# Optimization experiments

Hardware: AMD Instinct MI355X
Metric: run time of the kernel (lower is better)

The kernel has to match this reference:

```python
import jax, jax.numpy as jnp
import numpy as np

B, S, D = 2, 2048, 2048
H, DH, DR = 16, 128, 64
DC_KV, DC_Q = 512, 1536
ROPE_BASE = 10000.0


def _rope(t):
    """Apply rotate-half RoPE over the last dim of t: [B, S, H, DR]."""
    s, dr = t.shape[1], t.shape[-1]
    inv_freq = 1.0 / (ROPE_BASE ** (jnp.arange(0, dr, 2, dtype=jnp.float32) / dr))
    ang = jnp.arange(s, dtype=jnp.float32)[:, None] * inv_freq  # [S, DR/2]
    cos = jnp.tile(jnp.cos(ang), (1, 2))[None, :, None, :]  # [1,S,1,DR]
    sin = jnp.tile(jnp.sin(ang), (1, 2))[None, :, None, :]
    t1, t2 = jnp.split(t, 2, axis=-1)
    rot = jnp.concatenate([-t2, t1], axis=-1)
    return t * cos + rot * sin


def setup_inputs() -> dict:
    key = jax.random.key(0)
    ks = jax.random.split(key, 18)
    g = lambda k, shp: (jax.random.normal(k, shp, dtype=jnp.float32) * 0.02)
    return {
        "x": jax.random.normal(ks[0], (B, S, D), dtype=jnp.float32),
        "Wkd": g(ks[1], (DC_KV, D)),   "bkd": jnp.zeros((DC_KV,), jnp.float32),
        "Wqd": g(ks[2], (DC_Q, D)),    "bqd": jnp.zeros((DC_Q,), jnp.float32),
        "Wku": g(ks[3], (H * DH, DC_KV)), "bku": jnp.zeros((H * DH,), jnp.float32),
        "Wvu": g(ks[4], (H * DH, DC_KV)), "bvu": jnp.zeros((H * DH,), jnp.float32),
        "Wqu": g(ks[5], (H * DH, DC_Q)),  "bqu": jnp.zeros((H * DH,), jnp.float32),
        "Wkr": g(ks[6], (H * DR, D)),     "bkr": jnp.zeros((H * DR,), jnp.float32),
        "Wqr": g(ks[7], (H * DR, DC_Q)),  "bqr": jnp.zeros((H * DR,), jnp.float32),
        "Wo": g(ks[8], (D, H * DH)),      "bo": jnp.zeros((D,), jnp.float32),
    }


def reference(x, Wkd, bkd, Wqd, bqd, Wku, bku, Wvu, bvu, Wqu, bqu,
              Wkr, bkr, Wqr, bqr, Wo, bo):
    b, s, _ = x.shape
    # 1. Compress to latent spaces
    kv_c = x @ Wkd.T + bkd          # [B,S,DC_KV]
    q_c = x @ Wqd.T + bqd           # [B,S,DC_Q]
    # 2-3. Up-project content / value / rope features
    k_cnt = (kv_c @ Wku.T + bku).reshape(b, s, H, DH)
    v = (kv_c @ Wvu.T + bvu).reshape(b, s, H, DH)
    q_cnt = (q_c @ Wqu.T + bqu).reshape(b, s, H, DH)
    k_r = (x @ Wkr.T + bkr).reshape(b, s, H, DR)      # keys rope from input (eq. 3)
    q_r = (q_c @ Wqr.T + bqr).reshape(b, s, H, DR)    # query rope from latent (eq. 8)
    # 5. Partial RoPE: rotate position features, concat with content
    q_full = jnp.concatenate([q_cnt, _rope(q_r)], axis=-1)  # [B,S,H,DH+DR]
    k_full = jnp.concatenate([k_cnt, _rope(k_r)], axis=-1)
    # 7. Manual causal attention (mscale = 1)
    scale = 1.0 / jnp.sqrt(jnp.float32(DH + DR))
    scores = jnp.einsum("bqhd,bkhd->bhqk", q_full, k_full) * scale
    causal = jnp.tril(jnp.ones((s, s), dtype=bool))
    scores = jnp.where(causal[None, None], scores, jnp.float32(-1e9))
    probs = jax.nn.softmax(scores, axis=-1)
    attn = jnp.einsum("bhqk,bkhd->bqhd", probs, v).reshape(b, s, H * DH)
    # 9. Output projection
    return attn @ Wo.T + bo
```

## Files before the change

kernel.cpp:

```cpp
#include <hip/hip_runtime.h>
#include <stdint.h>
#include <stddef.h>

#define BB 2
#define SS 2048
#define DD 2048
#define HH 16
#define DHH 128
#define DRR 64
#define DCKV 512
#define DCQ 1536

typedef __attribute__((ext_vector_type(8))) short short8;
typedef __attribute__((ext_vector_type(4))) short short4v;
typedef __attribute__((ext_vector_type(4))) float f32x4;
typedef unsigned int u32;

__device__ __forceinline__ short f2bf(float x) {
  unsigned u = __float_as_uint(x);
  u += 0x7fffu + ((u >> 16) & 1u);
  return (short)(u >> 16);
}
__device__ __forceinline__ float bf2f(short s) {
  return __uint_as_float(((unsigned)(unsigned short)s) << 16);
}

#define BAR_NOVM() asm volatile("s_waitcnt lgkmcnt(0)\n\ts_barrier" ::: "memory")

__device__ __forceinline__ void gl2lds16(const short* g, short* l) {
  __builtin_amdgcn_global_load_lds(
      (const __attribute__((address_space(1))) u32*)g,
      (__attribute__((address_space(3))) u32*)l, 16, 0, 0);
}

__global__ __launch_bounds__(256) void cast_bf16_kernel(const float* __restrict__ in,
                                                        short* __restrict__ out, int n4) {
  int i = blockIdx.x * 256 + threadIdx.x;
  if (i >= n4) return;
  f32x4 f = ((const f32x4*)in)[i];
  short4v o;
  o[0] = f2bf(f[0]); o[1] = f2bf(f[1]); o[2] = f2bf(f[2]); o[3] = f2bf(f[3]);
  ((short4v*)out)[i] = o;
}

__global__ __launch_bounds__(256) void concat_bias_kernel(
    const float* bkd, const float* bqd, const float* bkr,
    const float* bqu, const float* bqr, const float* bku, const float* bvu,
    float* cb1, float* cb2, float* cb3) {
  int idx = blockIdx.x * 256 + threadIdx.x;
  if (idx < 3072) {
    cb1[idx] = idx < 512 ? bkd[idx] : (idx < 2048 ? bqd[idx - 512] : bkr[idx - 2048]);
  } else if (idx < 6144) {
    int j = idx - 3072;
    cb2[j] = j < 2048 ? bqu[j] : bqr[j - 2048];
  } else if (idx < 10240) {
    int j = idx - 6144;
    cb3[j] = j < 2048 ? bku[j] : bvu[j - 2048];
  }
}

template<int MODE>
__global__ __launch_bounds__(256) void gemm_bt(const short* __restrict__ A, int lda,
                                               const short* __restrict__ Bm, int ldb,
                                               const float* __restrict__ bias,
                                               void* __restrict__ Cout, void* __restrict__ out2,
                                               int M, int N, int K) {
  __shared__ __align__(16) short sA[128 * 32];
  __shared__ __align__(16) short sB[128 * 32];
  const int tid = threadIdx.x;
  const int w = tid >> 6, L = tid & 63, quad = L >> 4, lc = L & 15;
  const int wm = w >> 1, wn = w & 1;
  const int tm = blockIdx.x * 128, tn = blockIdx.y * 128;
  const int lrow = L >> 2, lch = (L & 3) * 8;
  f32x4 acc[4][4] = {};
  const int nk = K >> 5;
  for (int kt = 0; kt < nk; ++kt) {
    const int k0 = kt << 5;
    __syncthreads();
    {
      int sub = w * 2;
      gl2lds16(A + (size_t)(tm + sub * 16 + lrow) * lda + k0 + lch, &sA[sub * 512]);
      gl2lds16(A + (size_t)(tm + sub * 16 + 16 + lrow) * lda + k0 + lch, &sA[sub * 512 + 512]);
      gl2lds16(Bm + (size_t)(tn + sub * 16 + lrow) * ldb + k0 + lch, &sB[sub * 512]);
      gl2lds16(Bm + (size_t)(tn + sub * 16 + 16 + lrow) * ldb + k0 + lch, &sB[sub * 512 + 512]);
    }
    __syncthreads();
    short8 af[4], bfr[4];
#pragma unroll
    for (int ms = 0; ms < 4; ++ms)
      af[ms] = *(const short8*)&sA[(wm * 64 + ms * 16 + lc) * 32 + quad * 8];
#pragma unroll
    for (int ns = 0; ns < 4; ++ns)
      bfr[ns] = *(const short8*)&sB[(wn * 64 + ns * 16 + lc) * 32 + quad * 8];
#pragma unroll
    for (int ms = 0; ms < 4; ++ms)
#pragma unroll
      for (int ns = 0; ns < 4; ++ns)
        acc[ms][ns] = __builtin_amdgcn_mfma_f32_16x16x32_bf16(af[ms], bfr[ns], acc[ms][ns], 0, 0, 0);
  }
#pragma unroll
  for (int ms = 0; ms < 4; ++ms) {
    int row = tm + wm * 64 + ms * 16 + quad * 4;
#pragma unroll
    for (int ns = 0; ns < 4; ++ns) {
      int col = tn + wn * 64 + ns * 16 + lc;
      float bv = bias[col];
      if (MODE == 3 && col >= 2048) {
        int j = col - 2048, h_ = j >> 7, dh = j & 127;
        int b_ = row >> 11, s0 = row & 2047;
        short4v pk;
#pragma unroll
        for (int r = 0; r < 4; ++r) pk[r] = f2bf(acc[ms][ns][r] + bv);
        *(short4v*)((short*)out2 + (((size_t)(b_ * HH + h_)) * DHH + dh) * SS + s0) = pk;
      } else {
#pragma unroll
        for (int r = 0; r < 4; ++r) {
          float vv = acc[ms][ns][r] + bv;
          int rrow = row + r;
          if (MODE == 0)      ((short*)Cout)[(size_t)rrow * N + col] = f2bf(vv);
          else if (MODE == 1) ((float*)Cout)[(size_t)rrow * N + col] = vv;
          else {
            if (col < 2048) {
              int b_ = rrow >> 11, s_ = rrow & 2047, h_ = col >> 7, d_ = col & 127;
              ((short*)Cout)[(((size_t)(b_ * HH + h_)) * SS + s_) * 192 + d_] = f2bf(vv);
            } else {
              ((short*)out2)[(size_t)rrow * 1024 + (col - 2048)] = f2bf(vv);
            }
          }
        }
      }
    }
  }
}

__global__ __launch_bounds__(256) void rope_kernel(const short* __restrict__ rin,
                                                   int rstride, int roff,
                                                   short* __restrict__ full) {
  int idx = blockIdx.x * 256 + threadIdx.x;
  int i = idx & 31, h = (idx >> 5) & 15, s = (idx >> 9) & 2047, b = idx >> 20;
  const short* base = rin + ((size_t)(b * SS + s)) * rstride + roff + h * DRR;
  float t1 = bf2f(base[i]), t2 = bf2f(base[i + 32]);
  float invf = expf(-9.210340371976184f * (float)i * (1.0f / 32.0f));
  float ang = (float)s * invf;
  float c = cosf(ang), sn = sinf(ang);
  short* ob = full + (((size_t)(b * HH + h)) * SS + s) * 192 + 128;
  ob[i]      = f2bf(t1 * c - t2 * sn);
  ob[i + 32] = f2bf(t1 * sn + t2 * c);
}

__device__ __forceinline__ float quad_max(float v) {
  v = fmaxf(v, __shfl_xor(v, 1));
  v = fmaxf(v, __shfl_xor(v, 2));
  v = fmaxf(v, __shfl_xor(v, 4));
  v = fmaxf(v, __shfl_xor(v, 8));
  return v;
}
__device__ __forceinline__ float quad_sum(float v) {
  v += __shfl_xor(v, 1); v += __shfl_xor(v, 2);
  v += __shfl_xor(v, 4); v += __shfl_xor(v, 8);
  return v;
}

__global__ __launch_bounds__(256, 2) void mla_flash_kernel(const short* __restrict__ Qf,
                                                           const short* __restrict__ Kf,
                                                           const short* __restrict__ Vt,
                                                           float* __restrict__ Opart,
                                                           float* __restrict__ Mpart,
                                                           float* __restrict__ Lpart,
                                                           short* __restrict__ attn) {
  const int bid = blockIdx.x;
  const int g0 = (bid & 7) * 160 + (bid >> 3);
  const int bh = g0 / 40, xc = g0 - bh * 40;
  int qt, c;
  if (xc < 4)       { qt = xc;                  c = 0; }
  else if (xc < 12) { qt = 4 + ((xc - 4) >> 1);  c = (xc - 4) & 1; }
  else if (xc < 24) { qt = 8 + (xc - 12) / 3;    c = (xc - 12) % 3; }
  else              { qt = 12 + ((xc - 24) >> 2); c = (xc - 24) & 3; }
  const int nc = (qt + 4) >> 2;
  const int k8 = c * 8;
  const int klim = 2 * qt + 2;
  const int kend = (k8 + 8 < klim) ? k8 + 8 : klim;
  const int slot = bh * 40 + xc;

  const int h = bh & 15, b = bh >> 4;
  const int tid = threadIdx.x, w = tid >> 6, L = tid & 63, quad = L >> 4, lc = L & 15;
  __shared__ __align__(16) short sK[12288];
  __shared__ __align__(16) short sV[8192];
  __shared__ __align__(16) short Pf[8192];

  const short* Qb = Qf + ((size_t)bh) * SS * 192;
  const short* Kb = Kf + ((size_t)bh) * SS * 192;
  const short* Vb = Vt + ((size_t)bh) * DHH * SS;

  const int qrow0 = qt * 128 + w * 32;
  short8 qa[2][6];
#pragma unroll
  for (int ms = 0; ms < 2; ++ms)
#pragma unroll
    for (int kk = 0; kk < 6; ++kk)
      qa[ms][kk] = *(const short8*)(Qb + (size_t)(qrow0 + ms * 16 + lc) * 192 + kk * 32 + quad * 8);

  f32x4 O[2][8] = {};
  float mrow[2][4], lrow[2][4];
#pragma unroll
  for (int ms = 0; ms < 2; ++ms)
#pragma unroll
    for (int r = 0; r < 4; ++r) { mrow[ms][r] = -1e30f; lrow[ms][r] = 0.f; }

  const int srow_ = tid >> 2, sq_ = tid & 3;
  const int sslot = srow_ * 4 + (sq_ ^ ((srow_ >> 1) & 3));
  const int vrow_ = tid >> 3, vch_ = tid & 7;
  short8 g[6], gv[4];
#pragma unroll
  for (int i = 0; i < 6; ++i)
    g[i] = *(const short8*)(Kb + (size_t)(k8 * 64 + srow_) * 192 + i * 32 + sq_ * 8);
#pragma unroll
  for (int j = 0; j < 4; ++j)
    gv[j] = *(const short8*)(Vb + (size_t)(j * 32 + vrow_) * SS + k8 * 64 + vch_ * 8);

  for (int kt = k8; kt < kend; ++kt) {
    BAR_NOVM();
#pragma unroll
    for (int i = 0; i < 6; ++i)
      *(short8*)&sK[(i * 256 + sslot) * 8] = g[i];
#pragma unroll
    for (int j = 0; j < 4; ++j) {
      int row = j * 32 + vrow_;
      *(short8*)&sV[row * 64 + ((vch_ ^ (row & 7)) << 3)] = gv[j];
    }
    if (kt + 1 < kend) {
#pragma unroll
      for (int i = 0; i < 6; ++i)
        g[i] = *(const short8*)(Kb + (size_t)((kt + 1) * 64 + srow_) * 192 + i * 32 + sq_ * 8);
#pragma unroll
      for (int j = 0; j < 4; ++j)
        gv[j] = *(const short8*)(Vb + (size_t)(j * 32 + vrow_) * SS + (kt + 1) * 64 + vch_ * 8);
    }
    BAR_NOVM();
    f32x4 sc[2][4] = {};
#pragma unroll
    for (int kk = 0; kk < 6; ++kk)
#pragma unroll
      for (int ns = 0; ns < 4; ++ns) {
        int rr = ns * 16 + lc;
        short8 kb = *(const short8*)&sK[(kk * 256 + rr * 4 + (quad ^ ((rr >> 1) & 3))) * 8];
        sc[0][ns] = __builtin_amdgcn_mfma_f32_16x16x32_bf16(qa[0][kk], kb, sc[0][ns], 0, 0, 0);
        sc[1][ns] = __builtin_amdgcn_mfma_f32_16x16x32_bf16(qa[1][kk], kb, sc[1][ns], 0, 0, 0);
      }
    const float scale = 0.07216878364870322f;
#pragma unroll
    for (int ms = 0; ms < 2; ++ms)
#pragma unroll
      for (int ns = 0; ns < 4; ++ns)
#pragma unroll
        for (int r = 0; r < 4; ++r) {
          float vv = sc[ms][ns][r] * scale;
          if (kt * 64 + ns * 16 + lc > qrow0 + ms * 16 + quad * 4 + r) vv = -1e30f;
          sc[ms][ns][r] = vv;
        }
#pragma unroll
    for (int ms = 0; ms < 2; ++ms)
#pragma unroll
      for (int r = 0; r < 4; ++r) {
        float mx = fmaxf(fmaxf(sc[ms][0][r], sc[ms][1][r]), fmaxf(sc[ms][2][r], sc[ms][3][r]));
        mx = quad_max(mx);
        float mnew = fmaxf(mrow[ms][r], mx);
        float alpha = __expf(mrow[ms][r] - mnew);
        mrow[ms][r] = mnew;
        float ps = 0.f;
#pragma unroll
        for (int ns = 0; ns < 4; ++ns) {
          float p = __expf(sc[ms][ns][r] - mnew);
          sc[ms][ns][r] = p;
          ps += p;
        }
        ps = quad_sum(ps);
        lrow[ms][r] = lrow[ms][r] * alpha + ps;
#pragma unroll
        for (int n = 0; n < 8; ++n) O[ms][n][r] *= alpha;
      }
#pragma unroll
    for (int ms = 0; ms < 2; ++ms)
#pragma unroll
      for (int ns = 0; ns < 4; ++ns)
#pragma unroll
        for (int r = 0; r < 4; ++r) {
          int row = w * 32 + ms * 16 + quad * 4 + r;
          int col = ns * 16 + lc;
          Pf[row * 64 + (((col >> 3) ^ (row & 7)) << 3) + (col & 7)] = f2bf(sc[ms][ns][r]);
        }
#pragma unroll
    for (int kk2 = 0; kk2 < 2; ++kk2) {
      int r0 = w * 32 + lc, r1 = w * 32 + 16 + lc;
      short8 pa0 = *(const short8*)&Pf[r0 * 64 + (((kk2 * 4 + quad) ^ (r0 & 7)) << 3)];
      short8 pa1 = *(const short8*)&Pf[r1 * 64 + (((kk2 * 4 + quad) ^ (r1 & 7)) << 3)];
      short8 vb[8];
#pragma unroll
      for (int n = 0; n < 8; ++n) {
        int rr = n * 16 + lc;
        vb[n] = *(const short8*)&sV[rr * 64 + (((kk2 * 4 + quad) ^ (lc & 7)) << 3)];
      }
#pragma unroll
      for (int n = 0; n < 8; ++n) {
        O[0][n] = __builtin_amdgcn_mfma_f32_16x16x32_bf16(pa0, vb[n], O[0][n], 0, 0, 0);
        O[1][n] = __builtin_amdgcn_mfma_f32_16x16x32_bf16(pa1, vb[n], O[1][n], 0, 0, 0);
      }
    }
  }
  if (nc == 1) {
#pragma unroll
    for (int ms = 0; ms < 2; ++ms)
#pragma unroll
      for (int r = 0; r < 4; ++r) {
        float inv = 1.0f / lrow[ms][r];
        int srow = qt * 128 + w * 32 + ms * 16 + quad * 4 + r;
        short* dst = attn + ((size_t)b * SS + srow) * 2048 + h * 128;
#pragma unroll
        for (int n = 0; n < 8; ++n)
          dst[n * 16 + lc] = f2bf(O[ms][n][r] * inv);
      }
  } else {
    float* Ob = Opart + (size_t)slot * 16384;
#pragma unroll
    for (int ms = 0; ms < 2; ++ms)
#pragma unroll
      for (int r = 0; r < 4; ++r) {
        int row = w * 32 + ms * 16 + quad * 4 + r;
#pragma unroll
        for (int n = 0; n < 8; ++n)
          Ob[(size_t)row * 128 + n * 16 + lc] = O[ms][n][r];
      }
    if (lc == 0) {
#pragma unroll
      for (int ms = 0; ms < 2; ++ms)
#pragma unroll
        for (int r = 0; r < 4; ++r) {
          int row = w * 32 + ms * 16 + quad * 4 + r;
          Mpart[slot * 128 + row] = mrow[ms][r];
          Lpart[slot * 128 + row] = lrow[ms][r];
        }
    }
  }
}

__global__ __launch_bounds__(256) void combine_kernel(const float* __restrict__ Op,
                                                      const float* __restrict__ Mp,
                                                      const float* __restrict__ Lp,
                                                      short* __restrict__ attn) {
  int idx = blockIdx.x * 256 + threadIdx.x;
  int col = idx & 127;
  int r = (idx >> 7) & 127;
  int t = idx >> 14;
  int bh = t / 12, qt = (t - bh * 12) + 4;
  int nc = (qt + 4) >> 2;
  int cbase;
  if (qt < 8)       cbase = 4 + 2 * (qt - 4);
  else if (qt < 12) cbase = 12 + 3 * (qt - 8);
  else              cbase = 24 + 4 * (qt - 12);
  int slot0 = bh * 40 + cbase;
  float mc[4];
#pragma unroll
  for (int cc = 0; cc < 4; ++cc)
    mc[cc] = (cc < nc) ? Mp[(size_t)(slot0 + cc) * 128 + r] : -1e30f;
  float M = fmaxf(fmaxf(mc[0], mc[1]), fmaxf(mc[2], mc[3]));
  float den = 0.f, acc = 0.f;
#pragma unroll
  for (int cc = 0; cc < 4; ++cc) {
    if (cc < nc) {
      float e = __expf(mc[cc] - M);
      den += e * Lp[(size_t)(slot0 + cc) * 128 + r];
      acc += e * Op[(size_t)(slot0 + cc) * 16384 + (size_t)r * 128 + col];
    }
  }
  int b = bh >> 4, hh = bh & 15;
  int srow = qt * 128 + r;
  attn[((size_t)b * SS + srow) * 2048 + hh * 128 + col] = f2bf(acc / den);
}

extern "C" void kernel_launch(void* const* d_in, const int* in_sizes, int n_in,
                              void* d_out, int out_size, void* d_ws, size_t ws_size,
                              hipStream_t stream) {
  const float* x   = (const float*)d_in[0];
  const float* Wkd = (const float*)d_in[1];
  const float* bkd = (const float*)d_in[2];
  const float* Wqd = (const float*)d_in[3];
  const float* bqd = (const float*)d_in[4];
  const float* Wku = (const float*)d_in[5];
  const float* bku = (const float*)d_in[6];
  const float* Wvu = (const float*)d_in[7];
  const float* bvu = (const float*)d_in[8];
  const float* Wqu = (const float*)d_in[9];
  const float* bqu = (const float*)d_in[10];
  const float* Wkr = (const float*)d_in[11];
  const float* bkr = (const float*)d_in[12];
  const float* Wqr = (const float*)d_in[13];
  const float* bqr = (const float*)d_in[14];
  const float* Wo  = (const float*)d_in[15];
  const float* bo  = (const float*)d_in[16];

  char* ws = (char*)d_ws;
  size_t off = 0;
  auto alloc = [&](size_t elems, size_t esz) -> void* {
    void* p = (void*)(ws + off);
    off += elems * esz;
    off = (off + 255) & ~(size_t)255;
    return p;
  };
  const int MS = BB * SS;
  short* xb    = (short*)alloc((size_t)MS * DD, 2);
  short* cbuf  = (short*)alloc((size_t)MS * 3072, 2);
  short* qrbuf = (short*)alloc((size_t)MS * 1024, 2);
  short* vbuf  = (short*)alloc((size_t)MS * 2048, 2);
  short* w1    = (short*)alloc((size_t)3072 * 2048, 2);
  short* w2    = (short*)alloc((size_t)3072 * 1536, 2);
  short* w3    = (short*)alloc((size_t)4096 * 512, 2);
  short* wob   = (short*)alloc((size_t)2048 * 2048, 2);
  float* cb1   = (float*)alloc(3072, 4);
  float* cb2   = (float*)alloc(3072, 4);
  float* cb3   = (float*)alloc(4096, 4);
  short* qfull = (short*)alloc((size_t)BB * HH * SS * 192, 2);
  short* kfull = (short*)alloc((size_t)BB * HH * SS * 192, 2);
  short* vt    = (short*)alloc((size_t)BB * HH * DHH * SS, 2);
  short* attn  = (short*)alloc((size_t)MS * 2048, 2);
  if (off > ws_size) return;

  float* Opart = (float*)ws;
  float* Mpart = (float*)(ws + (size_t)1280 * 16384 * 4);
  float* Lpart = (float*)(ws + (size_t)1280 * 16384 * 4 + (size_t)1280 * 128 * 4);

  auto cast = [&](const float* src, short* dst, size_t n) {
    int n4 = (int)(n >> 2);
    cast_bf16_kernel<<<dim3((unsigned)((n4 + 255) / 256)), dim3(256), 0, stream>>>(src, dst, n4);
  };
  cast(x,   xb, (size_t)MS * DD);
  cast(Wkd, w1,                          (size_t)512 * 2048);
  cast(Wqd, w1 + (size_t)512 * 2048,     (size_t)1536 * 2048);
  cast(Wkr, w1 + (size_t)2048 * 2048,    (size_t)1024 * 2048);
  cast(Wqu, w2,                          (size_t)2048 * 1536);
  cast(Wqr, w2 + (size_t)2048 * 1536,    (size_t)1024 * 1536);
  cast(Wku, w3,                          (size_t)2048 * 512);
  cast(Wvu, w3 + (size_t)2048 * 512,     (size_t)2048 * 512);
  cast(Wo,  wob,                         (size_t)2048 * 2048);
  concat_bias_kernel<<<dim3(40), dim3(256), 0, stream>>>(bkd, bqd, bkr, bqu, bqr, bku, bvu,
                                                         cb1, cb2, cb3);

  dim3 blk(256);
  gemm_bt<0><<<dim3(32, 24), blk, 0, stream>>>(xb, DD, w1, DD, cb1, cbuf, nullptr,
                                               MS, 3072, DD);
  gemm_bt<2><<<dim3(32, 24), blk, 0, stream>>>(cbuf + 512, 3072, w2, DCQ, cb2, qfull, qrbuf,
                                               MS, 3072, DCQ);
  gemm_bt<3><<<dim3(32, 32), blk, 0, stream>>>(cbuf, 3072, w3, DCKV, cb3, kfull, vt,
                                               MS, 4096, DCKV);

  rope_kernel<<<dim3(BB * SS * HH * 32 / 256), blk, 0, stream>>>(qrbuf, 1024, 0, qfull);
  rope_kernel<<<dim3(BB * SS * HH * 32 / 256), blk, 0, stream>>>(cbuf, 3072, 2048, kfull);

  mla_flash_kernel<<<dim3(1280), blk, 0, stream>>>(qfull, kfull, vt, Opart, Mpart, Lpart, attn);
  combine_kernel<<<dim3(24576), blk, 0, stream>>>(Opart, Mpart, Lpart, attn);

  gemm_bt<1><<<dim3(32, 16), blk, 0, stream>>>(attn, DD, wob, DD, bo, d_out, nullptr,
                                               MS, DD, DD);
}
```

Before: 596.4 us.

## Fuse weight/input casts into one kernel and alias P buffer onto K LDS

Nine separate fp32-to-bf16 cast launches become a single kernel that picks its source and destination by index range, removing per-launch overhead and tail effects. The attention kernel also drops its dedicated P staging buffer and reuses the K tile's shared memory. A barrier is added so the K reads finish before P overwrites them. The smaller LDS footprint may allow more blocks per CU, at the cost of one extra barrier per iteration.

```diff
diff --git a/kernel.cpp b/kernel.cpp
--- a/kernel.cpp
+++ b/kernel.cpp
@@ -33,14 +33,29 @@
       (__attribute__((address_space(3))) u32*)l, 16, 0, 0);
 }
 
-__global__ __launch_bounds__(256) void cast_bf16_kernel(const float* __restrict__ in,
-                                                        short* __restrict__ out, int n4) {
+__global__ __launch_bounds__(256) void cast_all_kernel(
+    const float* __restrict__ x,   const float* __restrict__ Wkd,
+    const float* __restrict__ Wqd, const float* __restrict__ Wkr,
+    const float* __restrict__ Wqu, const float* __restrict__ Wqr,
+    const float* __restrict__ Wku, const float* __restrict__ Wvu,
+    const float* __restrict__ Wo,
+    short* __restrict__ xb, short* __restrict__ w1, short* __restrict__ w2,
+    short* __restrict__ w3, short* __restrict__ wob) {
   int i = blockIdx.x * 256 + threadIdx.x;
-  if (i >= n4) return;
-  f32x4 f = ((const f32x4*)in)[i];
+  const float* s; short* d; int j;
+  if (i < 2097152)      { s = x;   d = xb;                        j = i; }
+  else if (i < 2359296) { s = Wkd; d = w1;                        j = i - 2097152; }
+  else if (i < 3145728) { s = Wqd; d = w1 + (size_t)512 * 2048;   j = i - 2359296; }
+  else if (i < 3670016) { s = Wkr; d = w1 + (size_t)2048 * 2048;  j = i - 3145728; }
+  else if (i < 4456448) { s = Wqu; d = w2;                        j = i - 3670016; }
+  else if (i < 4849664) { s = Wqr; d = w2 + (size_t)2048 * 1536;  j = i - 4456448; }
+  else if (i < 5111808) { s = Wku; d = w3;                        j = i - 4849664; }
+  else if (i < 5373952) { s = Wvu; d = w3 + (size_t)2048 * 512;   j = i - 5111808; }
+  else                  { s = Wo;  d = wob;                       j = i - 5373952; }
+  f32x4 f = ((const f32x4*)s)[j];
   short4v o;
   o[0] = f2bf(f[0]); o[1] = f2bf(f[1]); o[2] = f2bf(f[2]); o[3] = f2bf(f[3]);
-  ((short4v*)out)[i] = o;
+  ((short4v*)d)[j] = o;
 }
 
 __global__ __launch_bounds__(256) void concat_bias_kernel(
@@ -186,7 +201,7 @@
   const int tid = threadIdx.x, w = tid >> 6, L = tid & 63, quad = L >> 4, lc = L & 15;
   __shared__ __align__(16) short sK[12288];
   __shared__ __align__(16) short sV[8192];
-  __shared__ __align__(16) short Pf[8192];
+  short* Pf = sK;
 
   const short* Qb = Qf + ((size_t)bh) * SS * 192;
   const short* Kb = Kf + ((size_t)bh) * SS * 192;
@@ -279,6 +294,7 @@
 #pragma unroll
         for (int n = 0; n < 8; ++n) O[ms][n][r] *= alpha;
       }
+    BAR_NOVM();
 #pragma unroll
     for (int ms = 0; ms < 2; ++ms)
 #pragma unroll
@@ -428,23 +444,12 @@
   float* Mpart = (float*)(ws + (size_t)1280 * 16384 * 4);
   float* Lpart = (float*)(ws + (size_t)1280 * 16384 * 4 + (size_t)1280 * 128 * 4);
 
-  auto cast = [&](const float* src, short* dst, size_t n) {
-    int n4 = (int)(n >> 2);
-    cast_bf16_kernel<<<dim3((unsigned)((n4 + 255) / 256)), dim3(256), 0, stream>>>(src, dst, n4);
-  };
-  cast(x,   xb, (size_t)MS * DD);
-  cast(Wkd, w1,                          (size_t)512 * 2048);
-  cast(Wqd, w1 + (size_t)512 * 2048,     (size_t)1536 * 2048);
-  cast(Wkr, w1 + (size_t)2048 * 2048,    (size_t)1024 * 2048);
-  cast(Wqu, w2,                          (size_t)2048 * 1536);
-  cast(Wqr, w2 + (size_t)2048 * 1536,    (size_t)1024 * 1536);
-  cast(Wku, w3,                          (size_t)2048 * 512);
-  cast(Wvu, w3 + (size_t)2048 * 512,     (size_t)2048 * 512);
-  cast(Wo,  wob,                         (size_t)2048 * 2048);
-  concat_bias_kernel<<<dim3(40), dim3(256), 0, stream>>>(bkd, bqd, bkr, bqu, bqr, bku, bvu,
-                                                         cb1, cb2, cb3);
-
   dim3 blk(256);
+  cast_all_kernel<<<dim3(25088), blk, 0, stream>>>(x, Wkd, Wqd, Wkr, Wqu, Wqr, Wku, Wvu, Wo,
+                                                   xb, w1, w2, w3, wob);
+  concat_bias_kernel<<<dim3(40), blk, 0, stream>>>(bkd, bqd, bkr, bqu, bqr, bku, bvu,
+                                                   cb1, cb2, cb3);
+
   gemm_bt<0><<<dim3(32, 24), blk, 0, stream>>>(xb, DD, w1, DD, cb1, cbuf, nullptr,
                                                MS, 3072, DD);
   gemm_bt<2><<<dim3(32, 24), blk, 0, stream>>>(cbuf + 512, 3072, w2, DCQ, cb2, qfull, qrbuf,
```

After: 607.9 us. About the same (+1.9%).
